# Kernel optimization log

Hardware: AMD Instinct MI355X
Metric: run time of the kernel (lower is better)

The kernel has to match this reference:

```python
import jax, jax.numpy as jnp
import numpy as np
from jax import lax

M = 8192  # number of candidate detections
C = 80    # number of classes (COCO)
MIN_CONF = 0.25
MIN_IOU = 0.45
VALID_CLASS_IDS = jnp.array([2, 3, 5, 7], dtype=jnp.int32)  # COCO vehicles


def setup_inputs() -> dict:
    key = jax.random.key(0)
    k1, k2, k3, k4, k5, k6, k7 = jax.random.split(key, 7)
    # boxes stored as (y1, x1, y2, x2) in input-image pixel space, guaranteed y1<y2, x1<x2
    y1 = jax.random.uniform(k1, (1, M)) * 600.0
    x1 = jax.random.uniform(k2, (1, M)) * 600.0
    h = jax.random.uniform(k3, (1, M)) * 120.0 + 4.0
    w = jax.random.uniform(k4, (1, M)) * 120.0 + 4.0
    boxes_raw = jnp.stack([y1, x1, y1 + h, x1 + w], axis=-1).astype(jnp.float32)  # [1,M,4]
    scores = jax.random.uniform(k5, (1, C, M), dtype=jnp.float32)  # [1,C,M]
    cls = jax.random.randint(k6, (1, M), 0, C, dtype=jnp.int32)
    idx = jax.random.randint(k7, (1, M), 0, M, dtype=jnp.int32)
    indices = jnp.stack([jnp.zeros_like(cls), cls, idx], axis=-1)  # [1,M,3]: (batch, class_id, box_idx)
    return {"boxes_raw": boxes_raw, "scores": scores, "indices": indices, "out_h": 640, "out_w": 640}


def _pairwise_iou(b):
    # b: [M,4] (x1,y1,x2,y2)
    x1, y1, x2, y2 = b[:, 0], b[:, 1], b[:, 2], b[:, 3]
    area = jnp.maximum(x2 - x1, 0.0) * jnp.maximum(y2 - y1, 0.0)  # [M]
    ix1 = jnp.maximum(x1[:, None], x1[None, :])
    iy1 = jnp.maximum(y1[:, None], y1[None, :])
    ix2 = jnp.minimum(x2[:, None], x2[None, :])
    iy2 = jnp.minimum(y2[:, None], y2[None, :])
    inter = jnp.maximum(ix2 - ix1, 0.0) * jnp.maximum(iy2 - iy1, 0.0)  # [M,M]
    return inter / (area[:, None] + area[None, :] - inter + 1e-9)


def _postprocess(boxes_raw, scores, indices, out_h, out_w):
    idxs = indices[0, :, 2]       # predicted-positive box indices [M]
    class_ids = indices[0, :, 1]  # class ids [M]
    conf = scores[0, class_ids, idxs]  # irregular gather [M]
    b = boxes_raw[0, idxs]  # [M,4] (y1,x1,y2,x2)
    # swap to (x1,y1,x2,y2) as in the original column permutation
    boxes = jnp.stack([b[:, 1], b[:, 0], b[:, 3], b[:, 2]], axis=-1)
    bounds = jnp.array([out_w, out_h, out_w, out_h], dtype=boxes.dtype)
    boxes = jnp.clip(boxes, 0.0, bounds)  # clip_boxes to output image size
    # confidence filter + class filter (as masks; static shapes)
    valid = (conf > MIN_CONF) & jnp.isin(class_ids, VALID_CLASS_IDS)
    # class-agnostic greedy NMS over valid detections
    s = jnp.where(valid, conf, -1.0)
    order = jnp.argsort(-s)  # descending score
    sb = boxes[order]
    sv = valid[order]
    iou = _pairwise_iou(sb)  # [M,M]
    rng = jnp.arange(M)

    def body(i, keep):
        suppress = keep[i] & (iou[i] > MIN_IOU) & (rng > i)
        return keep & ~suppress

    keep_sorted = lax.fori_loop(0, M, body, sv)
    keep = jnp.zeros((M,), dtype=bool).at[order].set(keep_sorted)
    boxes_out = boxes * keep[:, None].astype(boxes.dtype)
    conf_out = conf * keep.astype(conf.dtype)
    return boxes_out, conf_out, class_ids.astype(jnp.int64), keep


def reference(boxes_raw, scores, indices, out_h, out_w):
    return _postprocess(boxes_raw, scores, indices, out_h, out_w)
```

## Files before the change

kernel.cpp:

```cpp
#include <hip/hip_runtime.h>
#include <stdint.h>

#define M_BOXES 8192
#define MIN_CONF_F 0.25f
#define MIN_IOU_F 0.45f
#define VCAP 640
#define NW 10
#define NBLK 16

typedef unsigned long long u64;
typedef unsigned int u32;

#define WS_CNT    0
#define WS_WCNT   64
#define WS_VKEYS  1024
#define WS_SKEY   66560
#define WS_SBOX   71680
#define WS_SAREA  81920
#define WS_SUP    84480
#define WS_NEED   135680

__device__ inline float scalar_to_float(const int* p) {
    int v = p[0];
    if (v > 0 && v < (1 << 20)) return (float)v;
    return __int_as_float(v);
}

__device__ inline u64 rl64(u64 v, int b) {
    u32 lo = (u32)__builtin_amdgcn_readlane((int)(u32)v, b);
    u32 hi = (u32)__builtin_amdgcn_readlane((int)(u32)(v >> 32), b);
    return ((u64)hi << 32) | lo;
}

__device__ inline u64 wave_or64(u64 v) {
    #pragma unroll
    for (int o = 32; o > 0; o >>= 1) {
        int lo = __shfl_xor((int)(u32)v, o, 64);
        int hi = __shfl_xor((int)(u32)(v >> 32), o, 64);
        v |= ((u64)(u32)hi << 32) | (u32)lo;
    }
    return v;
}

__device__ inline void grid_bar(int* c, int nblk) {
    __syncthreads();
    if (threadIdx.x == 0) {
        __hip_atomic_fetch_add(c, 1, __ATOMIC_ACQ_REL, __HIP_MEMORY_SCOPE_AGENT);
        while (__hip_atomic_load(c, __ATOMIC_ACQUIRE, __HIP_MEMORY_SCOPE_AGENT) < nblk)
            __builtin_amdgcn_s_sleep(1);
    }
    __syncthreads();
}

__global__ __launch_bounds__(512) void kA_gather(
    const float* __restrict__ scores, const int* __restrict__ indices,
    float* __restrict__ out, u64* __restrict__ vkeys, int* __restrict__ wcnt,
    int* __restrict__ cnt)
{
    int tid = threadIdx.x;
    int i = blockIdx.x * 512 + tid;
    if (i == 0) { cnt[0] = 0; cnt[1] = 0; }
    int cls = indices[3 * i + 1];
    int idx = indices[3 * i + 2];
    float conf = scores[cls * M_BOXES + idx];
    *reinterpret_cast<float4*>(out + 4 * i) = make_float4(0.f, 0.f, 0.f, 0.f);
    out[4 * M_BOXES + i] = 0.f;
    out[5 * M_BOXES + i] = (float)cls;
    out[6 * M_BOXES + i] = 0.f;
    bool valid = (conf > MIN_CONF_F) &&
                 (cls == 2 || cls == 3 || cls == 5 || cls == 7);
    u64 mask = __ballot(valid);
    int lane = tid & 63;
    int wid = i >> 6;
    if (valid) {
        int pos = (int)__popcll(mask & ((1ull << lane) - 1ull));
        u64 key = ((u64)(~__float_as_uint(conf)) << 32)
                | ((u64)(u32)i << 13) | (u64)(u32)idx;
        vkeys[(wid << 6) + pos] = key;
    }
    if (lane == 0) wcnt[wid] = (int)__popcll(mask);
}

__global__ __launch_bounds__(512) void kMEGA(
    const float* __restrict__ boxes_raw, const int* __restrict__ p_out_h,
    const int* __restrict__ p_out_w, float* __restrict__ out,
    const u64* __restrict__ vkeys, const int* __restrict__ wcnt,
    u64* __restrict__ skey, float4* __restrict__ sbox,
    float* __restrict__ sarea, u64* __restrict__ sup, int* __restrict__ cnt)
{
    __shared__ int pre_s[129];
    __shared__ u64 tkey[VCAP];
    __shared__ u64 live_s[NW];
    int tid = threadIdx.x;
    int widx = tid >> 6, lane = tid & 63;

    if (tid < 64) {
        int cA = wcnt[tid], cB = wcnt[64 + tid];
        int sA = cA, sB = cB;
        #pragma unroll
        for (int o = 1; o < 64; o <<= 1) {
            int t = __shfl_up(sA, o, 64); if (tid >= o) sA += t;
            int u = __shfl_up(sB, o, 64); if (tid >= o) sB += u;
        }
        int totA = __shfl(sA, 63, 64);
        int totB = __shfl(sB, 63, 64);
        pre_s[tid] = sA - cA;
        pre_s[64 + tid] = totA + sB - cB;
        if (tid == 0) pre_s[128] = totA + totB;
    }
    __syncthreads();
    int V = pre_s[128];
    if (V > VCAP) V = VCAP;

    if (V > 0) {
        for (int s = tid; s < V; s += 512) {
            int lo = 0, hi = 128;
            #pragma unroll
            for (int st = 0; st < 7; ++st) {
                int mid = (lo + hi) >> 1;
                if (pre_s[mid] <= s) lo = mid; else hi = mid;
            }
            tkey[s] = vkeys[(lo << 6) + (s - pre_s[lo])];
        }
        __syncthreads();

        float W = scalar_to_float(p_out_w);
        float H = scalar_to_float(p_out_h);
        int spb = (V + NBLK - 1) / NBLK;
        int s0 = blockIdx.x * spb;
        int send = s0 + spb; if (send > V) send = V;
        for (int s = s0 + widx; s < send; s += 8) {
            u64 k = tkey[s];
            int r = 0;
            for (int j = lane; j < V; j += 64) r += (tkey[j] < k) ? 1 : 0;
            #pragma unroll
            for (int o = 1; o < 64; o <<= 1) r += __shfl_xor(r, o, 64);
            if (lane == 0) {
                int bidx = (int)(k & 0x1FFFull);
                float4 b = *reinterpret_cast<const float4*>(boxes_raw + 4 * bidx);
                float4 c4;
                c4.x = fminf(fmaxf(b.y, 0.f), W);
                c4.y = fminf(fmaxf(b.x, 0.f), H);
                c4.z = fminf(fmaxf(b.w, 0.f), W);
                c4.w = fminf(fmaxf(b.z, 0.f), H);
                skey[r] = k;
                sbox[r] = c4;
                sarea[r] = fmaxf(c4.z - c4.x, 0.f) * fmaxf(c4.w - c4.y, 0.f);
            }
        }
    }
    grid_bar(&cnt[0], NBLK);

    if (V > 0) {
        int nw = (V + 63) >> 6;
        int nbi = (V + 7) >> 3;
        int ntask = nbi * nw;
        int gwave = blockIdx.x * 8 + widx;
        for (int t = gwave; t < ntask; t += NBLK * 8) {
            int bi = t / nw;
            int w = t - bi * nw;
            int i0 = bi << 3;
            int j = (w << 6) + lane;
            bool jv = j < V;
            float4 bj = jv ? sbox[j] : make_float4(0.f, 0.f, 0.f, 0.f);
            float aj = jv ? sarea[j] : 0.f;
            int rend = V - i0; if (rend > 8) rend = 8;
            for (int r = 0; r < rend; ++r) {
                int i = i0 + r;
                float4 bi4 = sbox[i];
                float ai = sarea[i];
                bool p = false;
                if (jv && j > i) {
                    float ix1 = fmaxf(bi4.x, bj.x);
                    float iy1 = fmaxf(bi4.y, bj.y);
                    float ix2 = fminf(bi4.z, bj.z);
                    float iy2 = fminf(bi4.w, bj.w);
                    float inter = fmaxf(ix2 - ix1, 0.f) * fmaxf(iy2 - iy1, 0.f);
                    float iou = inter / (ai + aj - inter + 1e-9f);
                    p = iou > MIN_IOU_F;
                }
                u64 bits = __ballot(p);
                if (lane == 0) sup[i * NW + w] = bits;
            }
        }
    }
    grid_bar(&cnt[1], NBLK);

    if (blockIdx.x != 0 || V <= 0) return;
    int nw = (V + 63) >> 6;
    if (tid < 64) {
        u64 live[NW], supp[NW];
        #pragma unroll
        for (int w = 0; w < NW; ++w) {
            int c = V - (w << 6);
            live[w] = (c >= 64) ? ~0ull : (c > 0 ? ((1ull << c) - 1ull) : 0ull);
            supp[w] = 0ull;
        }
        u64 rowA[NW], rowB[NW];
        {
            bool rv = lane < V;
            #pragma unroll
            for (int w = 0; w < NW; ++w)
                rowA[w] = (rv && w < nw) ? sup[lane * NW + w] : 0ull;
        }
        auto step = [&](u64 (&rc)[NW], u64 (&rn)[NW], int ci) {
            int rI = ((ci + 1) << 6) + lane;
            bool rv = (ci + 1) < nw && rI < V;
            #pragma unroll
            for (int w = 0; w < NW; ++w)
                rn[w] = (rv && w >= ci + 1 && w < nw) ? sup[rI * NW + w] : 0ull;
            u64 rw = 0, cur = 0;
            #pragma unroll
            for (int w = 0; w < NW; ++w)
                if (w == ci) { rw = rc[w]; cur = live[w] & ~supp[w]; }
            #pragma unroll
            for (int b = 0; b < 64; ++b) {
                u64 rb = rl64(rw, b);
                u64 nxt = cur & ~rb;
                cur = ((cur >> b) & 1ull) ? nxt : cur;
            }
            #pragma unroll
            for (int w = 0; w < NW; ++w) if (w == ci) live[w] = cur;
            #pragma unroll
            for (int w2 = 0; w2 < NW; ++w2)
                if (w2 > ci && w2 < nw) {
                    u64 mine = ((cur >> lane) & 1ull) ? rc[w2] : 0ull;
                    supp[w2] |= wave_or64(mine);
                }
        };
        int ci = 0;
        while (ci < nw) {
            step(rowA, rowB, ci); ++ci;
            if (ci < nw) { step(rowB, rowA, ci); ++ci; }
        }
        #pragma unroll
        for (int w = 0; w < NW; ++w) live_s[w] = live[w];
    }
    __syncthreads();
    for (int s = tid; s < V; s += 512) {
        if ((live_s[s >> 6] >> (s & 63)) & 1ull) {
            u64 k = skey[s];
            u32 orig = (u32)((k >> 13) & 0x1FFFull);
            float conf = __uint_as_float(~(u32)(k >> 32));
            float4 b = sbox[s];
            *reinterpret_cast<float4*>(out + 4 * orig) = b;
            out[4 * M_BOXES + orig] = conf;
            out[6 * M_BOXES + orig] = 1.0f;
        }
    }
}

__global__ __launch_bounds__(256) void fb_gather(
    const float* __restrict__ boxes_raw, const float* __restrict__ scores,
    const int* __restrict__ indices, const int* __restrict__ p_out_h,
    const int* __restrict__ p_out_w, float* __restrict__ out,
    u64* __restrict__ vkeys, float4* __restrict__ vboxes,
    int* __restrict__ vcount)
{
    int i = blockIdx.x * blockDim.x + threadIdx.x;
    if (i >= M_BOXES) return;
    int cls = indices[3 * i + 1];
    int idx = indices[3 * i + 2];
    float conf = scores[cls * M_BOXES + idx];
    *reinterpret_cast<float4*>(out + 4 * i) = make_float4(0.f, 0.f, 0.f, 0.f);
    out[4 * M_BOXES + i] = 0.f;
    out[5 * M_BOXES + i] = (float)cls;
    out[6 * M_BOXES + i] = 0.f;
    bool valid = (conf > MIN_CONF_F) &&
                 (cls == 2 || cls == 3 || cls == 5 || cls == 7);
    if (valid) {
        float4 b = *reinterpret_cast<const float4*>(boxes_raw + 4 * idx);
        float W = scalar_to_float(p_out_w);
        float H = scalar_to_float(p_out_h);
        float4 c;
        c.x = fminf(fmaxf(b.y, 0.f), W);
        c.y = fminf(fmaxf(b.x, 0.f), H);
        c.z = fminf(fmaxf(b.w, 0.f), W);
        c.w = fminf(fmaxf(b.z, 0.f), H);
        int p = atomicAdd(vcount, 1);
        if (p < VCAP) {
            vkeys[p] = ((u64)(~__float_as_uint(conf)) << 32) | (u32)i;
            vboxes[p] = c;
        }
    }
}

__global__ __launch_bounds__(1024) void fb_nms(
    float* __restrict__ out, const u64* __restrict__ vkeys,
    const float4* __restrict__ vboxes, const int* __restrict__ vcount)
{
    __shared__ u64 tkey[VCAP];
    __shared__ u64 skey[VCAP];
    __shared__ float4 sbox[VCAP];
    __shared__ unsigned char keepb[VCAP];
    int tid = threadIdx.x;
    int V = *vcount;
    if (V > VCAP) V = VCAP;
    if (V <= 0) return;
    for (int s = tid; s < V; s += 1024) tkey[s] = vkeys[s];
    __syncthreads();
    for (int s = tid; s < V; s += 1024) {
        u64 k = tkey[s];
        int r = 0;
        for (int j = 0; j < V; ++j) r += (tkey[j] < k);
        skey[r] = k;
        sbox[r] = vboxes[s];
    }
    __syncthreads();
    for (int s = tid; s < V; s += 1024) keepb[s] = 1;
    __syncthreads();
    for (int i = 0; i < V; ++i) {
        if (keepb[i]) {
            float4 bi = sbox[i];
            float ai = fmaxf(bi.z - bi.x, 0.f) * fmaxf(bi.w - bi.y, 0.f);
            for (int s = i + 1 + tid; s < V; s += 1024) {
                if (keepb[s]) {
                    float4 bj = sbox[s];
                    float aj = fmaxf(bj.z - bj.x, 0.f) * fmaxf(bj.w - bj.y, 0.f);
                    float ix1 = fmaxf(bi.x, bj.x);
                    float iy1 = fmaxf(bi.y, bj.y);
                    float ix2 = fminf(bi.z, bj.z);
                    float iy2 = fminf(bi.w, bj.w);
                    float inter = fmaxf(ix2 - ix1, 0.f) * fmaxf(iy2 - iy1, 0.f);
                    float iou = inter / (ai + aj - inter + 1e-9f);
                    if (iou > MIN_IOU_F) keepb[s] = 0;
                }
            }
        }
        __syncthreads();
    }
    for (int s = tid; s < V; s += 1024) {
        if (keepb[s]) {
            u64 k = skey[s];
            u32 orig = (u32)(k & 0xFFFFFFFFull);
            float conf = __uint_as_float(~(u32)(k >> 32));
            float4 b = sbox[s];
            *reinterpret_cast<float4*>(out + 4 * orig) = b;
            out[4 * M_BOXES + orig] = conf;
            out[6 * M_BOXES + orig] = 1.0f;
        }
    }
}

extern "C" void kernel_launch(void* const* d_in, const int* in_sizes, int n_in,
                              void* d_out, int out_size, void* d_ws, size_t ws_size,
                              hipStream_t stream) {
    const float* boxes_raw = (const float*)d_in[0];
    const float* scores    = (const float*)d_in[1];
    const int*   indices   = (const int*)d_in[2];
    const int*   p_out_h   = (const int*)d_in[3];
    const int*   p_out_w   = (const int*)d_in[4];
    float* out = (float*)d_out;
    char* ws = (char*)d_ws;

    if (ws_size >= WS_NEED) {
        int*    cnt   = (int*)(ws + WS_CNT);
        int*    wcnt  = (int*)(ws + WS_WCNT);
        u64*    vkeys = (u64*)(ws + WS_VKEYS);
        u64*    skey  = (u64*)(ws + WS_SKEY);
        float4* sbox  = (float4*)(ws + WS_SBOX);
        float*  sarea = (float*)(ws + WS_SAREA);
        u64*    sup   = (u64*)(ws + WS_SUP);

        kA_gather<<<M_BOXES / 512, 512, 0, stream>>>(
            scores, indices, out, vkeys, wcnt, cnt);
        kMEGA<<<NBLK, 512, 0, stream>>>(
            boxes_raw, p_out_h, p_out_w, out, vkeys, wcnt,
            skey, sbox, sarea, sup, cnt);
    } else {
        int*    vcount = (int*)ws;
        u64*    vkeys  = (u64*)(ws + 16);
        float4* vboxes = (float4*)(ws + 16 + VCAP * sizeof(u64));
        hipMemsetAsync(d_ws, 0, 16, stream);
        fb_gather<<<M_BOXES / 256, 256, 0, stream>>>(
            boxes_raw, scores, indices, p_out_h, p_out_w, out,
            vkeys, vboxes, vcount);
        fb_nms<<<1, 1024, 0, stream>>>(out, vkeys, vboxes, vcount);
    }
}
```

Measured before the change: 37.67 us.

## Fuse gather and NMS into one kernel with redundant per-block compaction and sort

Merges the gather kernel into the NMS kernel. Each of the 16 blocks redundantly reads all 8192 candidates, compacts and rank-sorts the valid keys in shared memory, then computes its share of the suppression bitmask. This removes one kernel launch, the first grid barrier, and the global workspace round-trips for keys, boxes and areas. Block 0 waits on per-block flags before running the greedy bitmask pass, and resets the flags at the end so the next call starts clean. The cost is that every block repeats the full gather and rank sort.

```diff
diff --git a/kernel.cpp b/kernel.cpp
--- a/kernel.cpp
+++ b/kernel.cpp
@@ -7,18 +7,15 @@
 #define VCAP 640
 #define NW 10
 #define NBLK 16
+#define NCHUNK 16
+#define FLAG_MAGIC 0x5EEDF00D
 
 typedef unsigned long long u64;
 typedef unsigned int u32;
 
-#define WS_CNT    0
-#define WS_WCNT   64
-#define WS_VKEYS  1024
-#define WS_SKEY   66560
-#define WS_SBOX   71680
-#define WS_SAREA  81920
-#define WS_SUP    84480
-#define WS_NEED   135680
+#define WS_FLAGS  0
+#define WS_SUP    64
+#define WS_NEED   (64 + VCAP * NW * 8)
 
 __device__ inline float scalar_to_float(const int* p) {
     int v = p[0];
@@ -42,60 +39,49 @@
     return v;
 }
 
-__device__ inline void grid_bar(int* c, int nblk) {
-    __syncthreads();
-    if (threadIdx.x == 0) {
-        __hip_atomic_fetch_add(c, 1, __ATOMIC_ACQ_REL, __HIP_MEMORY_SCOPE_AGENT);
-        while (__hip_atomic_load(c, __ATOMIC_ACQUIRE, __HIP_MEMORY_SCOPE_AGENT) < nblk)
-            __builtin_amdgcn_s_sleep(1);
-    }
-    __syncthreads();
-}
-
-__global__ __launch_bounds__(512) void kA_gather(
-    const float* __restrict__ scores, const int* __restrict__ indices,
-    float* __restrict__ out, u64* __restrict__ vkeys, int* __restrict__ wcnt,
-    int* __restrict__ cnt)
+__global__ __launch_bounds__(512) void kONE(
+    const float* __restrict__ boxes_raw, const float* __restrict__ scores,
+    const int* __restrict__ indices, const int* __restrict__ p_out_h,
+    const int* __restrict__ p_out_w, float* __restrict__ out,
+    u64* __restrict__ sup, int* __restrict__ flags)
 {
-    int tid = threadIdx.x;
-    int i = blockIdx.x * 512 + tid;
-    if (i == 0) { cnt[0] = 0; cnt[1] = 0; }
-    int cls = indices[3 * i + 1];
-    int idx = indices[3 * i + 2];
-    float conf = scores[cls * M_BOXES + idx];
-    *reinterpret_cast<float4*>(out + 4 * i) = make_float4(0.f, 0.f, 0.f, 0.f);
-    out[4 * M_BOXES + i] = 0.f;
-    out[5 * M_BOXES + i] = (float)cls;
-    out[6 * M_BOXES + i] = 0.f;
-    bool valid = (conf > MIN_CONF_F) &&
-                 (cls == 2 || cls == 3 || cls == 5 || cls == 7);
-    u64 mask = __ballot(valid);
-    int lane = tid & 63;
-    int wid = i >> 6;
-    if (valid) {
-        int pos = (int)__popcll(mask & ((1ull << lane) - 1ull));
-        u64 key = ((u64)(~__float_as_uint(conf)) << 32)
-                | ((u64)(u32)i << 13) | (u64)(u32)idx;
-        vkeys[(wid << 6) + pos] = key;
-    }
-    if (lane == 0) wcnt[wid] = (int)__popcll(mask);
-}
-
-__global__ __launch_bounds__(512) void kMEGA(
-    const float* __restrict__ boxes_raw, const int* __restrict__ p_out_h,
-    const int* __restrict__ p_out_w, float* __restrict__ out,
-    const u64* __restrict__ vkeys, const int* __restrict__ wcnt,
-    u64* __restrict__ skey, float4* __restrict__ sbox,
-    float* __restrict__ sarea, u64* __restrict__ sup, int* __restrict__ cnt)
-{
+    __shared__ int wcnt_s[128];
     __shared__ int pre_s[129];
     __shared__ u64 tkey[VCAP];
+    __shared__ u64 skey_s[VCAP];
+    __shared__ float4 sbox_s[VCAP];
+    __shared__ float sarea_s[VCAP];
     __shared__ u64 live_s[NW];
-    int tid = threadIdx.x;
+
+    int tid = threadIdx.x, b = blockIdx.x;
     int widx = tid >> 6, lane = tid & 63;
 
+    u64 keys[NCHUNK];
+    u32 validbits = 0;
+    #pragma unroll
+    for (int c = 0; c < NCHUNK; ++c) {
+        int i = (c << 9) + tid;
+        int cls = indices[3 * i + 1];
+        int idx = indices[3 * i + 2];
+        float conf = scores[cls * M_BOXES + idx];
+        if (c == b) {
+            *reinterpret_cast<float4*>(out + 4 * i) = make_float4(0.f, 0.f, 0.f, 0.f);
+            out[4 * M_BOXES + i] = 0.f;
+            out[5 * M_BOXES + i] = (float)cls;
+            out[6 * M_BOXES + i] = 0.f;
+        }
+        bool valid = (conf > MIN_CONF_F) &&
+                     (cls == 2 || cls == 3 || cls == 5 || cls == 7);
+        u64 mask = __ballot(valid);
+        keys[c] = ((u64)(~__float_as_uint(conf)) << 32)
+                | ((u64)(u32)i << 13) | (u64)(u32)idx;
+        validbits |= (valid ? 1u : 0u) << c;
+        if (lane == 0) wcnt_s[(c << 3) + widx] = (int)__popcll(mask);
+    }
+    __syncthreads();
+
     if (tid < 64) {
-        int cA = wcnt[tid], cB = wcnt[64 + tid];
+        int cA = wcnt_s[tid], cB = wcnt_s[64 + tid];
         int sA = cA, sB = cB;
         #pragma unroll
         for (int o = 1; o < 64; o <<= 1) {
@@ -112,24 +98,22 @@
     int V = pre_s[128];
     if (V > VCAP) V = VCAP;
 
+    #pragma unroll
+    for (int c = 0; c < NCHUNK; ++c) {
+        bool valid = (validbits >> c) & 1u;
+        u64 mask = __ballot(valid);
+        if (valid) {
+            int pos = (int)__popcll(mask & ((1ull << lane) - 1ull));
+            int p = pre_s[(c << 3) + widx] + pos;
+            if (p < VCAP) tkey[p] = keys[c];
+        }
+    }
+    __syncthreads();
+
     if (V > 0) {
-        for (int s = tid; s < V; s += 512) {
-            int lo = 0, hi = 128;
-            #pragma unroll
-            for (int st = 0; st < 7; ++st) {
-                int mid = (lo + hi) >> 1;
-                if (pre_s[mid] <= s) lo = mid; else hi = mid;
-            }
-            tkey[s] = vkeys[(lo << 6) + (s - pre_s[lo])];
-        }
-        __syncthreads();
-
         float W = scalar_to_float(p_out_w);
         float H = scalar_to_float(p_out_h);
-        int spb = (V + NBLK - 1) / NBLK;
-        int s0 = blockIdx.x * spb;
-        int send = s0 + spb; if (send > V) send = V;
-        for (int s = s0 + widx; s < send; s += 8) {
+        for (int s = widx; s < V; s += 8) {
             u64 k = tkey[s];
             int r = 0;
             for (int j = lane; j < V; j += 64) r += (tkey[j] < k) ? 1 : 0;
@@ -137,38 +121,38 @@
             for (int o = 1; o < 64; o <<= 1) r += __shfl_xor(r, o, 64);
             if (lane == 0) {
                 int bidx = (int)(k & 0x1FFFull);
-                float4 b = *reinterpret_cast<const float4*>(boxes_raw + 4 * bidx);
+                float4 bb = *reinterpret_cast<const float4*>(boxes_raw + 4 * bidx);
                 float4 c4;
-                c4.x = fminf(fmaxf(b.y, 0.f), W);
-                c4.y = fminf(fmaxf(b.x, 0.f), H);
-                c4.z = fminf(fmaxf(b.w, 0.f), W);
-                c4.w = fminf(fmaxf(b.z, 0.f), H);
-                skey[r] = k;
-                sbox[r] = c4;
-                sarea[r] = fmaxf(c4.z - c4.x, 0.f) * fmaxf(c4.w - c4.y, 0.f);
-            }
-        }
-    }
-    grid_bar(&cnt[0], NBLK);
+                c4.x = fminf(fmaxf(bb.y, 0.f), W);
+                c4.y = fminf(fmaxf(bb.x, 0.f), H);
+                c4.z = fminf(fmaxf(bb.w, 0.f), W);
+                c4.w = fminf(fmaxf(bb.z, 0.f), H);
+                skey_s[r] = k;
+                sbox_s[r] = c4;
+                sarea_s[r] = fmaxf(c4.z - c4.x, 0.f) * fmaxf(c4.w - c4.y, 0.f);
+            }
+        }
+    }
+    __syncthreads();
 
     if (V > 0) {
         int nw = (V + 63) >> 6;
         int nbi = (V + 7) >> 3;
         int ntask = nbi * nw;
-        int gwave = blockIdx.x * 8 + widx;
-        for (int t = gwave; t < ntask; t += NBLK * 8) {
+        int gw = (b << 3) + widx;
+        for (int t = gw; t < ntask; t += NBLK * 8) {
             int bi = t / nw;
             int w = t - bi * nw;
             int i0 = bi << 3;
             int j = (w << 6) + lane;
             bool jv = j < V;
-            float4 bj = jv ? sbox[j] : make_float4(0.f, 0.f, 0.f, 0.f);
-            float aj = jv ? sarea[j] : 0.f;
+            float4 bj = jv ? sbox_s[j] : make_float4(0.f, 0.f, 0.f, 0.f);
+            float aj = jv ? sarea_s[j] : 0.f;
             int rend = V - i0; if (rend > 8) rend = 8;
             for (int r = 0; r < rend; ++r) {
                 int i = i0 + r;
-                float4 bi4 = sbox[i];
-                float ai = sarea[i];
+                float4 bi4 = sbox_s[i];
+                float ai = sarea_s[i];
                 bool p = false;
                 if (jv && j > i) {
                     float ix1 = fmaxf(bi4.x, bj.x);
@@ -184,70 +168,95 @@
             }
         }
     }
-    grid_bar(&cnt[1], NBLK);
-
-    if (blockIdx.x != 0 || V <= 0) return;
-    int nw = (V + 63) >> 6;
-    if (tid < 64) {
-        u64 live[NW], supp[NW];
-        #pragma unroll
-        for (int w = 0; w < NW; ++w) {
-            int c = V - (w << 6);
-            live[w] = (c >= 64) ? ~0ull : (c > 0 ? ((1ull << c) - 1ull) : 0ull);
-            supp[w] = 0ull;
-        }
-        u64 rowA[NW], rowB[NW];
-        {
-            bool rv = lane < V;
+
+    __syncthreads();
+    if (tid == 0) {
+        __threadfence();
+        __hip_atomic_store(&flags[b], FLAG_MAGIC, __ATOMIC_RELEASE,
+                           __HIP_MEMORY_SCOPE_AGENT);
+    }
+    if (b != 0) return;
+
+    if (tid == 0) {
+        bool ok;
+        do {
+            ok = true;
+            for (int q = 0; q < NBLK; ++q)
+                ok &= (__hip_atomic_load(&flags[q], __ATOMIC_ACQUIRE,
+                                         __HIP_MEMORY_SCOPE_AGENT) == FLAG_MAGIC);
+            if (!ok) __builtin_amdgcn_s_sleep(1);
+        } while (!ok);
+        __threadfence();
+    }
+    __syncthreads();
+
+    if (V > 0) {
+        int nw = (V + 63) >> 6;
+        if (tid < 64) {
+            u64 live[NW], supp[NW];
             #pragma unroll
-            for (int w = 0; w < NW; ++w)
-                rowA[w] = (rv && w < nw) ? sup[lane * NW + w] : 0ull;
-        }
-        auto step = [&](u64 (&rc)[NW], u64 (&rn)[NW], int ci) {
-            int rI = ((ci + 1) << 6) + lane;
-            bool rv = (ci + 1) < nw && rI < V;
+            for (int w = 0; w < NW; ++w) {
+                int c = V - (w << 6);
+                live[w] = (c >= 64) ? ~0ull : (c > 0 ? ((1ull << c) - 1ull) : 0ull);
+                supp[w] = 0ull;
+            }
+            u64 rowA[NW], rowB[NW];
+            {
+                bool rv = lane < V;
+                #pragma unroll
+                for (int w = 0; w < NW; ++w)
+                    rowA[w] = (rv && w < nw) ? sup[lane * NW + w] : 0ull;
+            }
+            auto step = [&](u64 (&rc)[NW], u64 (&rn)[NW], int ci) {
+                int rI = ((ci + 1) << 6) + lane;
+                bool rv = (ci + 1) < nw && rI < V;
+                #pragma unroll
+                for (int w = 0; w < NW; ++w)
+                    rn[w] = (rv && w >= ci + 1 && w < nw) ? sup[rI * NW + w] : 0ull;
+                u64 rw = 0, cur = 0;
+                #pragma unroll
+                for (int w = 0; w < NW; ++w)
+                    if (w == ci) { rw = rc[w]; cur = live[w] & ~supp[w]; }
+                #pragma unroll
+                for (int bb = 0; bb < 64; ++bb) {
+                    u64 rb = rl64(rw, bb);
+                    u64 nxt = cur & ~rb;
+                    cur = ((cur >> bb) & 1ull) ? nxt : cur;
+                }
+                #pragma unroll
+                for (int w = 0; w < NW; ++w) if (w == ci) live[w] = cur;
+                #pragma unroll
+                for (int w2 = 0; w2 < NW; ++w2)
+                    if (w2 > ci && w2 < nw) {
+                        u64 mine = ((cur >> lane) & 1ull) ? rc[w2] : 0ull;
+                        supp[w2] |= wave_or64(mine);
+                    }
+            };
+            int ci = 0;
+            while (ci < nw) {
+                step(rowA, rowB, ci); ++ci;
+                if (ci < nw) { step(rowB, rowA, ci); ++ci; }
+            }
             #pragma unroll
-            for (int w = 0; w < NW; ++w)
-                rn[w] = (rv && w >= ci + 1 && w < nw) ? sup[rI * NW + w] : 0ull;
-            u64 rw = 0, cur = 0;
-            #pragma unroll
-            for (int w = 0; w < NW; ++w)
-                if (w == ci) { rw = rc[w]; cur = live[w] & ~supp[w]; }
-            #pragma unroll
-            for (int b = 0; b < 64; ++b) {
-                u64 rb = rl64(rw, b);
-                u64 nxt = cur & ~rb;
-                cur = ((cur >> b) & 1ull) ? nxt : cur;
-            }
-            #pragma unroll
-            for (int w = 0; w < NW; ++w) if (w == ci) live[w] = cur;
-            #pragma unroll
-            for (int w2 = 0; w2 < NW; ++w2)
-                if (w2 > ci && w2 < nw) {
-                    u64 mine = ((cur >> lane) & 1ull) ? rc[w2] : 0ull;
-                    supp[w2] |= wave_or64(mine);
-                }
-        };
-        int ci = 0;
-        while (ci < nw) {
-            step(rowA, rowB, ci); ++ci;
-            if (ci < nw) { step(rowB, rowA, ci); ++ci; }
-        }
-        #pragma unroll
-        for (int w = 0; w < NW; ++w) live_s[w] = live[w];
-    }
-    __syncthreads();
-    for (int s = tid; s < V; s += 512) {
-        if ((live_s[s >> 6] >> (s & 63)) & 1ull) {
-            u64 k = skey[s];
-            u32 orig = (u32)((k >> 13) & 0x1FFFull);
-            float conf = __uint_as_float(~(u32)(k >> 32));
-            float4 b = sbox[s];
-            *reinterpret_cast<float4*>(out + 4 * orig) = b;
-            out[4 * M_BOXES + orig] = conf;
-            out[6 * M_BOXES + orig] = 1.0f;
-        }
-    }
+            for (int w = 0; w < NW; ++w) live_s[w] = live[w];
+        }
+        __syncthreads();
+        for (int s = tid; s < V; s += 512) {
+            if ((live_s[s >> 6] >> (s & 63)) & 1ull) {
+                u64 k = skey_s[s];
+                u32 orig = (u32)((k >> 13) & 0x1FFFull);
+                float conf = __uint_as_float(~(u32)(k >> 32));
+                float4 bb = sbox_s[s];
+                *reinterpret_cast<float4*>(out + 4 * orig) = bb;
+                out[4 * M_BOXES + orig] = conf;
+                out[6 * M_BOXES + orig] = 1.0f;
+            }
+        }
+    }
+
+    if (tid < NBLK)
+        __hip_atomic_store(&flags[tid], 0, __ATOMIC_RELEASE,
+                           __HIP_MEMORY_SCOPE_AGENT);
 }
 
 __global__ __launch_bounds__(256) void fb_gather(
@@ -269,14 +278,14 @@
     bool valid = (conf > MIN_CONF_F) &&
                  (cls == 2 || cls == 3 || cls == 5 || cls == 7);
     if (valid) {
-        float4 b = *reinterpret_cast<const float4*>(boxes_raw + 4 * idx);
+        float4 bb = *reinterpret_cast<const float4*>(boxes_raw + 4 * idx);
         float W = scalar_to_float(p_out_w);
         float H = scalar_to_float(p_out_h);
         float4 c;
-        c.x = fminf(fmaxf(b.y, 0.f), W);
-        c.y = fminf(fmaxf(b.x, 0.f), H);
-        c.z = fminf(fmaxf(b.w, 0.f), W);
-        c.w = fminf(fmaxf(b.z, 0.f), H);
+        c.x = fminf(fmaxf(bb.y, 0.f), W);
+        c.y = fminf(fmaxf(bb.x, 0.f), H);
+        c.z = fminf(fmaxf(bb.w, 0.f), W);
+        c.w = fminf(fmaxf(bb.z, 0.f), H);
         int p = atomicAdd(vcount, 1);
         if (p < VCAP) {
             vkeys[p] = ((u64)(~__float_as_uint(conf)) << 32) | (u32)i;
@@ -334,8 +343,8 @@
             u64 k = skey[s];
             u32 orig = (u32)(k & 0xFFFFFFFFull);
             float conf = __uint_as_float(~(u32)(k >> 32));
-            float4 b = sbox[s];
-            *reinterpret_cast<float4*>(out + 4 * orig) = b;
+            float4 bb = sbox[s];
+            *reinterpret_cast<float4*>(out + 4 * orig) = bb;
             out[4 * M_BOXES + orig] = conf;
             out[6 * M_BOXES + orig] = 1.0f;
         }
@@ -354,19 +363,10 @@
     char* ws = (char*)d_ws;
 
     if (ws_size >= WS_NEED) {
-        int*    cnt   = (int*)(ws + WS_CNT);
-        int*    wcnt  = (int*)(ws + WS_WCNT);
-        u64*    vkeys = (u64*)(ws + WS_VKEYS);
-        u64*    skey  = (u64*)(ws + WS_SKEY);
-        float4* sbox  = (float4*)(ws + WS_SBOX);
-        float*  sarea = (float*)(ws + WS_SAREA);
-        u64*    sup   = (u64*)(ws + WS_SUP);
-
-        kA_gather<<<M_BOXES / 512, 512, 0, stream>>>(
-            scores, indices, out, vkeys, wcnt, cnt);
-        kMEGA<<<NBLK, 512, 0, stream>>>(
-            boxes_raw, p_out_h, p_out_w, out, vkeys, wcnt,
-            skey, sbox, sarea, sup, cnt);
+        int* flags = (int*)(ws + WS_FLAGS);
+        u64* sup   = (u64*)(ws + WS_SUP);
+        kONE<<<NBLK, 512, 0, stream>>>(
+            boxes_raw, scores, indices, p_out_h, p_out_w, out, sup, flags);
     } else {
         int*    vcount = (int*)ws;
         u64*    vkeys  = (u64*)(ws + 16);
```

After: 61.14 us. 62.3% more time.

## Fuse gather kernel into persistent NMS kernel with per-block flag barriers

Applied to the files above, without the earlier changes.

The separate gather kernel is folded into the 16-block persistent kernel, so each block first gathers its 512 candidates and then proceeds into rank/sort, IoU mask and greedy resolve. The counter-based grid barrier is replaced by per-block magic flags that every block polls, and block 0 resets them at the end. This removes one kernel launch and the dependency gap between launches. In exchange, the first call relies on the workspace flags starting non-magic, and each block now does the gather serially.

```diff
diff --git a/kernel.cpp b/kernel.cpp
--- a/kernel.cpp
+++ b/kernel.cpp
@@ -7,12 +7,15 @@
 #define VCAP 640
 #define NW 10
 #define NBLK 16
+#define FLAG_MAGIC 0x5EEDF00D
 
 typedef unsigned long long u64;
 typedef unsigned int u32;
 
-#define WS_CNT    0
-#define WS_WCNT   64
+#define WS_FA     0
+#define WS_FB     64
+#define WS_FC     128
+#define WS_WCNT   192
 #define WS_VKEYS  1024
 #define WS_SKEY   66560
 #define WS_SBOX   71680
@@ -42,57 +45,60 @@
     return v;
 }
 
-__device__ inline void grid_bar(int* c, int nblk) {
+__device__ inline void flag_bar_all(int* f, int b) {
     __syncthreads();
     if (threadIdx.x == 0) {
-        __hip_atomic_fetch_add(c, 1, __ATOMIC_ACQ_REL, __HIP_MEMORY_SCOPE_AGENT);
-        while (__hip_atomic_load(c, __ATOMIC_ACQUIRE, __HIP_MEMORY_SCOPE_AGENT) < nblk)
+        __threadfence();
+        __hip_atomic_store(&f[b], FLAG_MAGIC, __ATOMIC_RELEASE,
+                           __HIP_MEMORY_SCOPE_AGENT);
+    }
+    if (threadIdx.x < NBLK) {
+        while (__hip_atomic_load(&f[threadIdx.x], __ATOMIC_ACQUIRE,
+                                 __HIP_MEMORY_SCOPE_AGENT) != FLAG_MAGIC)
             __builtin_amdgcn_s_sleep(1);
     }
     __syncthreads();
-}
-
-__global__ __launch_bounds__(512) void kA_gather(
-    const float* __restrict__ scores, const int* __restrict__ indices,
-    float* __restrict__ out, u64* __restrict__ vkeys, int* __restrict__ wcnt,
-    int* __restrict__ cnt)
-{
-    int tid = threadIdx.x;
-    int i = blockIdx.x * 512 + tid;
-    if (i == 0) { cnt[0] = 0; cnt[1] = 0; }
-    int cls = indices[3 * i + 1];
-    int idx = indices[3 * i + 2];
-    float conf = scores[cls * M_BOXES + idx];
-    *reinterpret_cast<float4*>(out + 4 * i) = make_float4(0.f, 0.f, 0.f, 0.f);
-    out[4 * M_BOXES + i] = 0.f;
-    out[5 * M_BOXES + i] = (float)cls;
-    out[6 * M_BOXES + i] = 0.f;
-    bool valid = (conf > MIN_CONF_F) &&
-                 (cls == 2 || cls == 3 || cls == 5 || cls == 7);
-    u64 mask = __ballot(valid);
-    int lane = tid & 63;
-    int wid = i >> 6;
-    if (valid) {
-        int pos = (int)__popcll(mask & ((1ull << lane) - 1ull));
-        u64 key = ((u64)(~__float_as_uint(conf)) << 32)
-                | ((u64)(u32)i << 13) | (u64)(u32)idx;
-        vkeys[(wid << 6) + pos] = key;
-    }
-    if (lane == 0) wcnt[wid] = (int)__popcll(mask);
-}
-
-__global__ __launch_bounds__(512) void kMEGA(
-    const float* __restrict__ boxes_raw, const int* __restrict__ p_out_h,
+    __threadfence();
+}
+
+__global__ __launch_bounds__(512) void kFUSED(
+    const float* __restrict__ boxes_raw, const float* __restrict__ scores,
+    const int* __restrict__ indices, const int* __restrict__ p_out_h,
     const int* __restrict__ p_out_w, float* __restrict__ out,
-    const u64* __restrict__ vkeys, const int* __restrict__ wcnt,
+    u64* __restrict__ vkeys, int* __restrict__ wcnt,
     u64* __restrict__ skey, float4* __restrict__ sbox,
-    float* __restrict__ sarea, u64* __restrict__ sup, int* __restrict__ cnt)
+    float* __restrict__ sarea, u64* __restrict__ sup,
+    int* __restrict__ fA, int* __restrict__ fB, int* __restrict__ fC)
 {
     __shared__ int pre_s[129];
     __shared__ u64 tkey[VCAP];
     __shared__ u64 live_s[NW];
-    int tid = threadIdx.x;
+
+    int tid = threadIdx.x, b = blockIdx.x;
     int widx = tid >> 6, lane = tid & 63;
+
+    {
+        int i = (b << 9) + tid;
+        int cls = indices[3 * i + 1];
+        int idx = indices[3 * i + 2];
+        float conf = scores[cls * M_BOXES + idx];
+        *reinterpret_cast<float4*>(out + 4 * i) = make_float4(0.f, 0.f, 0.f, 0.f);
+        out[4 * M_BOXES + i] = 0.f;
+        out[5 * M_BOXES + i] = (float)cls;
+        out[6 * M_BOXES + i] = 0.f;
+        bool valid = (conf > MIN_CONF_F) &&
+                     (cls == 2 || cls == 3 || cls == 5 || cls == 7);
+        u64 mask = __ballot(valid);
+        int wid = i >> 6;
+        if (valid) {
+            int pos = (int)__popcll(mask & ((1ull << lane) - 1ull));
+            u64 key = ((u64)(~__float_as_uint(conf)) << 32)
+                    | ((u64)(u32)i << 13) | (u64)(u32)idx;
+            vkeys[(wid << 6) + pos] = key;
+        }
+        if (lane == 0) wcnt[wid] = (int)__popcll(mask);
+    }
+    flag_bar_all(fA, b);
 
     if (tid < 64) {
         int cA = wcnt[tid], cB = wcnt[64 + tid];
@@ -127,7 +133,7 @@
         float W = scalar_to_float(p_out_w);
         float H = scalar_to_float(p_out_h);
         int spb = (V + NBLK - 1) / NBLK;
-        int s0 = blockIdx.x * spb;
+        int s0 = b * spb;
         int send = s0 + spb; if (send > V) send = V;
         for (int s = s0 + widx; s < send; s += 8) {
             u64 k = tkey[s];
@@ -137,26 +143,26 @@
             for (int o = 1; o < 64; o <<= 1) r += __shfl_xor(r, o, 64);
             if (lane == 0) {
                 int bidx = (int)(k & 0x1FFFull);
-                float4 b = *reinterpret_cast<const float4*>(boxes_raw + 4 * bidx);
+                float4 bb = *reinterpret_cast<const float4*>(boxes_raw + 4 * bidx);
                 float4 c4;
-                c4.x = fminf(fmaxf(b.y, 0.f), W);
-                c4.y = fminf(fmaxf(b.x, 0.f), H);
-                c4.z = fminf(fmaxf(b.w, 0.f), W);
-                c4.w = fminf(fmaxf(b.z, 0.f), H);
+                c4.x = fminf(fmaxf(bb.y, 0.f), W);
+                c4.y = fminf(fmaxf(bb.x, 0.f), H);
+                c4.z = fminf(fmaxf(bb.w, 0.f), W);
+                c4.w = fminf(fmaxf(bb.z, 0.f), H);
                 skey[r] = k;
                 sbox[r] = c4;
                 sarea[r] = fmaxf(c4.z - c4.x, 0.f) * fmaxf(c4.w - c4.y, 0.f);
             }
         }
     }
-    grid_bar(&cnt[0], NBLK);
+    flag_bar_all(fB, b);
 
     if (V > 0) {
         int nw = (V + 63) >> 6;
         int nbi = (V + 7) >> 3;
         int ntask = nbi * nw;
-        int gwave = blockIdx.x * 8 + widx;
-        for (int t = gwave; t < ntask; t += NBLK * 8) {
+        int gw = (b << 3) + widx;
+        for (int t = gw; t < ntask; t += NBLK * 8) {
             int bi = t / nw;
             int w = t - bi * nw;
             int i0 = bi << 3;
@@ -184,69 +190,90 @@
             }
         }
     }
-    grid_bar(&cnt[1], NBLK);
-
-    if (blockIdx.x != 0 || V <= 0) return;
-    int nw = (V + 63) >> 6;
-    if (tid < 64) {
-        u64 live[NW], supp[NW];
-        #pragma unroll
-        for (int w = 0; w < NW; ++w) {
-            int c = V - (w << 6);
-            live[w] = (c >= 64) ? ~0ull : (c > 0 ? ((1ull << c) - 1ull) : 0ull);
-            supp[w] = 0ull;
-        }
-        u64 rowA[NW], rowB[NW];
-        {
-            bool rv = lane < V;
+
+    __syncthreads();
+    if (tid == 0) {
+        __threadfence();
+        __hip_atomic_store(&fC[b], FLAG_MAGIC, __ATOMIC_RELEASE,
+                           __HIP_MEMORY_SCOPE_AGENT);
+    }
+    if (b != 0) return;
+    if (tid < NBLK) {
+        while (__hip_atomic_load(&fC[tid], __ATOMIC_ACQUIRE,
+                                 __HIP_MEMORY_SCOPE_AGENT) != FLAG_MAGIC)
+            __builtin_amdgcn_s_sleep(1);
+    }
+    __syncthreads();
+    __threadfence();
+
+    if (V > 0) {
+        int nw = (V + 63) >> 6;
+        if (tid < 64) {
+            u64 live[NW], supp[NW];
             #pragma unroll
-            for (int w = 0; w < NW; ++w)
-                rowA[w] = (rv && w < nw) ? sup[lane * NW + w] : 0ull;
-        }
-        auto step = [&](u64 (&rc)[NW], u64 (&rn)[NW], int ci) {
-            int rI = ((ci + 1) << 6) + lane;
-            bool rv = (ci + 1) < nw && rI < V;
+            for (int w = 0; w < NW; ++w) {
+                int c = V - (w << 6);
+                live[w] = (c >= 64) ? ~0ull : (c > 0 ? ((1ull << c) - 1ull) : 0ull);
+                supp[w] = 0ull;
+            }
+            u64 rowA[NW], rowB[NW];
+            {
+                bool rv = lane < V;
+                #pragma unroll
+                for (int w = 0; w < NW; ++w)
+                    rowA[w] = (rv && w < nw) ? sup[lane * NW + w] : 0ull;
+            }
+            auto step = [&](u64 (&rc)[NW], u64 (&rn)[NW], int ci) {
+                int rI = ((ci + 1) << 6) + lane;
+                bool rv = (ci + 1) < nw && rI < V;
+                #pragma unroll
+                for (int w = 0; w < NW; ++w)
+                    rn[w] = (rv && w >= ci + 1 && w < nw) ? sup[rI * NW + w] : 0ull;
+                u64 rw = 0, cur = 0;
+                #pragma unroll
+                for (int w = 0; w < NW; ++w)
+                    if (w == ci) { rw = rc[w]; cur = live[w] & ~supp[w]; }
+                #pragma unroll
+                for (int bb = 0; bb < 64; ++bb) {
+                    u64 rb = rl64(rw, bb);
+                    u64 nxt = cur & ~rb;
+                    cur = ((cur >> bb) & 1ull) ? nxt : cur;
+                }
+                #pragma unroll
+                for (int w = 0; w < NW; ++w) if (w == ci) live[w] = cur;
+                #pragma unroll
+                for (int w2 = 0; w2 < NW; ++w2)
+                    if (w2 > ci && w2 < nw) {
+                        u64 mine = ((cur >> lane) & 1ull) ? rc[w2] : 0ull;
+                        supp[w2] |= wave_or64(mine);
+                    }
+            };
+            int ci = 0;
+            while (ci < nw) {
+                step(rowA, rowB, ci); ++ci;
+                if (ci < nw) { step(rowB, rowA, ci); ++ci; }
+            }
             #pragma unroll
-            for (int w = 0; w < NW; ++w)
-                rn[w] = (rv && w >= ci + 1 && w < nw) ? sup[rI * NW + w] : 0ull;
-            u64 rw = 0, cur = 0;
-            #pragma unroll
-            for (int w = 0; w < NW; ++w)
-                if (w == ci) { rw = rc[w]; cur = live[w] & ~supp[w]; }
-            #pragma unroll
-            for (int b = 0; b < 64; ++b) {
-                u64 rb = rl64(rw, b);
-                u64 nxt = cur & ~rb;
-                cur = ((cur >> b) & 1ull) ? nxt : cur;
-            }
-            #pragma unroll
-            for (int w = 0; w < NW; ++w) if (w == ci) live[w] = cur;
-            #pragma unroll
-            for (int w2 = 0; w2 < NW; ++w2)
-                if (w2 > ci && w2 < nw) {
-                    u64 mine = ((cur >> lane) & 1ull) ? rc[w2] : 0ull;
-                    supp[w2] |= wave_or64(mine);
-                }
-        };
-        int ci = 0;
-        while (ci < nw) {
-            step(rowA, rowB, ci); ++ci;
-            if (ci < nw) { step(rowB, rowA, ci); ++ci; }
-        }
-        #pragma unroll
-        for (int w = 0; w < NW; ++w) live_s[w] = live[w];
-    }
-    __syncthreads();
-    for (int s = tid; s < V; s += 512) {
-        if ((live_s[s >> 6] >> (s & 63)) & 1ull) {
-            u64 k = skey[s];
-            u32 orig = (u32)((k >> 13) & 0x1FFFull);
-            float conf = __uint_as_float(~(u32)(k >> 32));
-            float4 b = sbox[s];
-            *reinterpret_cast<float4*>(out + 4 * orig) = b;
-            out[4 * M_BOXES + orig] = conf;
-            out[6 * M_BOXES + orig] = 1.0f;
-        }
+            for (int w = 0; w < NW; ++w) live_s[w] = live[w];
+        }
+        __syncthreads();
+        for (int s = tid; s < V; s += 512) {
+            if ((live_s[s >> 6] >> (s & 63)) & 1ull) {
+                u64 k = skey[s];
+                u32 orig = (u32)((k >> 13) & 0x1FFFull);
+                float conf = __uint_as_float(~(u32)(k >> 32));
+                float4 bb = sbox[s];
+                *reinterpret_cast<float4*>(out + 4 * orig) = bb;
+                out[4 * M_BOXES + orig] = conf;
+                out[6 * M_BOXES + orig] = 1.0f;
+            }
+        }
+    }
+
+    if (tid < NBLK) {
+        __hip_atomic_store(&fA[tid], 0, __ATOMIC_RELEASE, __HIP_MEMORY_SCOPE_AGENT);
+        __hip_atomic_store(&fB[tid], 0, __ATOMIC_RELEASE, __HIP_MEMORY_SCOPE_AGENT);
+        __hip_atomic_store(&fC[tid], 0, __ATOMIC_RELEASE, __HIP_MEMORY_SCOPE_AGENT);
     }
 }
 
@@ -269,14 +296,14 @@
     bool valid = (conf > MIN_CONF_F) &&
                  (cls == 2 || cls == 3 || cls == 5 || cls == 7);
     if (valid) {
-        float4 b = *reinterpret_cast<const float4*>(boxes_raw + 4 * idx);
+        float4 bb = *reinterpret_cast<const float4*>(boxes_raw + 4 * idx);
         float W = scalar_to_float(p_out_w);
         float H = scalar_to_float(p_out_h);
         float4 c;
-        c.x = fminf(fmaxf(b.y, 0.f), W);
-        c.y = fminf(fmaxf(b.x, 0.f), H);
-        c.z = fminf(fmaxf(b.w, 0.f), W);
-        c.w = fminf(fmaxf(b.z, 0.f), H);
+        c.x = fminf(fmaxf(bb.y, 0.f), W);
+        c.y = fminf(fmaxf(bb.x, 0.f), H);
+        c.z = fminf(fmaxf(bb.w, 0.f), W);
+        c.w = fminf(fmaxf(bb.z, 0.f), H);
         int p = atomicAdd(vcount, 1);
         if (p < VCAP) {
             vkeys[p] = ((u64)(~__float_as_uint(conf)) << 32) | (u32)i;
@@ -334,8 +361,8 @@
             u64 k = skey[s];
             u32 orig = (u32)(k & 0xFFFFFFFFull);
             float conf = __uint_as_float(~(u32)(k >> 32));
-            float4 b = sbox[s];
-            *reinterpret_cast<float4*>(out + 4 * orig) = b;
+            float4 bb = sbox[s];
+            *reinterpret_cast<float4*>(out + 4 * orig) = bb;
             out[4 * M_BOXES + orig] = conf;
             out[6 * M_BOXES + orig] = 1.0f;
         }
@@ -354,7 +381,9 @@
     char* ws = (char*)d_ws;
 
     if (ws_size >= WS_NEED) {
-        int*    cnt   = (int*)(ws + WS_CNT);
+        int*    fA    = (int*)(ws + WS_FA);
+        int*    fB    = (int*)(ws + WS_FB);
+        int*    fC    = (int*)(ws + WS_FC);
         int*    wcnt  = (int*)(ws + WS_WCNT);
         u64*    vkeys = (u64*)(ws + WS_VKEYS);
         u64*    skey  = (u64*)(ws + WS_SKEY);
@@ -362,11 +391,9 @@
         float*  sarea = (float*)(ws + WS_SAREA);
         u64*    sup   = (u64*)(ws + WS_SUP);
 
-        kA_gather<<<M_BOXES / 512, 512, 0, stream>>>(
-            scores, indices, out, vkeys, wcnt, cnt);
-        kMEGA<<<NBLK, 512, 0, stream>>>(
-            boxes_raw, p_out_h, p_out_w, out, vkeys, wcnt,
-            skey, sbox, sarea, sup, cnt);
+        kFUSED<<<NBLK, 512, 0, stream>>>(
+            boxes_raw, scores, indices, p_out_h, p_out_w, out,
+            vkeys, wcnt, skey, sbox, sarea, sup, fA, fB, fC);
     } else {
         int*    vcount = (int*)ws;
         u64*    vkeys  = (u64*)(ws + 16);
```

Result: slower. 41.25 us (+9.5%).
